# Kernel tuning notes

Measured on AMD Instinct MI355X. Metric: run time of the kernel, lower is better.

Reference implementation:

```python
import jax, jax.numpy as jnp
import numpy as np

# BQQ block dims: Y_sign (p,j,k,m,l), Z_sign (p,j,k,l,n); in=k*n=4096, out=j*m=4096
P, J, K, M, L, N = 2, 32, 32, 128, 16, 128
ACT_BITS = 8  # activation quantization bits


def setup_inputs() -> dict:
    key = jax.random.key(0)
    ks = jax.random.split(key, 7)
    x = jax.random.normal(ks[0], (1, 512, K * N), dtype=jnp.float32)
    # sign matrices in {-1,+1}
    Y_sign = jnp.where(jax.random.normal(ks[1], (P, J, K, M, L)) >= 0, 1.0, -1.0).astype(jnp.float32)
    Z_sign = jnp.where(jax.random.normal(ks[2], (P, J, K, L, N)) >= 0, 1.0, -1.0).astype(jnp.float32)
    # per-block positive scales (abs-mean in the original, so strictly > 0)
    Y_scale = jax.random.uniform(ks[3], (P, J, K, 1, 1), minval=0.01, maxval=0.1, dtype=jnp.float32)
    Z_scale = jax.random.uniform(ks[4], (P, J, K, 1, 1), minval=0.01, maxval=0.1, dtype=jnp.float32)
    A = jax.random.normal(ks[5], (P, J, K, 4), dtype=jnp.float32) * 0.1
    bias = jax.random.normal(ks[6], (J * M,), dtype=jnp.float32) * 0.1
    return {"input": x, "Y_sign": Y_sign, "Z_sign": Z_sign,
            "Y_scale": Y_scale, "Z_scale": Z_scale, "A": A, "bias": bias}


def reference(input, Y_sign, Z_sign, Y_scale, Z_scale, A, bias):
    # --- activation quantization (act_bits = 8, simple round, no STE) ---
    qmax = float(2 ** (ACT_BITS - 1) - 1)  # 127
    x_max = jnp.max(input)
    x_min = jnp.min(input)
    act_scale = jnp.maximum((x_max - x_min) / (2.0 * qmax), 1e-8)
    X = jnp.clip(jnp.round(input / act_scale), -qmax, qmax) * act_scale

    # --- dequantize sign * scale ---
    Y_q = Y_sign * Y_scale  # (p,j,k,m,l)
    Z_q = Z_sign * Z_scale  # (p,j,k,l,n)

    orig_shape = X.shape[:-1]
    X_kn = X.reshape(-1, K, N)  # (B,k,n)

    # chained block einsums
    T = jnp.einsum('bkn,pjkln->bpjkl', X_kn, Z_q)          # (B,p,j,k,l)
    core = jnp.einsum('pjkml,bpjkl->bpjkm', Y_q, T)        # (B,p,j,k,m)

    # quant_bias=True correction terms: A[...,0..3] = (a,b,c,d)
    out1 = jnp.einsum('bpjkm,pjk->bjm', core, A[..., 0])

    Y_sum = Y_q.sum(axis=-1)                               # (p,j,k,m)
    B_coef = jnp.einsum('pjk,pjkm->jkm', A[..., 1], Y_sum)
    Sx = X_kn.sum(axis=-1)                                 # (B,k)
    out2 = jnp.einsum('bk,jkm->bjm', Sx, B_coef)

    Zs = Z_q.sum(axis=-2)                                  # (p,j,k,n)
    Tz = jnp.einsum('bkn,pjkn->bpjk', X_kn, Zs)
    out3 = jnp.einsum('bpjk,pjk->bj', Tz, A[..., 2])

    D_coef = A[..., 3].sum(axis=0)                         # (j,k)
    out4 = jnp.einsum('bk,jk->bj', Sx, D_coef)

    out_bjm = out1 + out2 + (out3 + out4)[:, :, None]      # (B,j,m)
    out_2d = out_bjm.reshape(-1, J * M) + bias
    return out_2d.reshape(*orig_shape, J * M)
```

## Files before the change

kernel.cpp:

```cpp
#include <hip/hip_runtime.h>
#include <hip/hip_bf16.h>

typedef __attribute__((ext_vector_type(4))) float f32x4;
typedef __attribute__((ext_vector_type(8))) short bf16x8;

#define GLOBAL_AS __attribute__((address_space(1)))
#define LDS_AS __attribute__((address_space(3)))

static __device__ __forceinline__ unsigned short f2bf(float f) {
  __hip_bfloat16 h = __float2bfloat16(f);
  return __builtin_bit_cast(unsigned short, h);
}
static __device__ __forceinline__ float bf2f(unsigned short u) {
  unsigned int v = ((unsigned int)u) << 16;
  return __builtin_bit_cast(float, v);
}
static __device__ __forceinline__ void load_lds16(const void* g, void* l) {
  __builtin_amdgcn_global_load_lds((GLOBAL_AS void*)g, (LDS_AS void*)l, 16, 0, 0);
}

__global__ __launch_bounds__(256) void k_minmax_part(const float* __restrict__ x,
                                                     float* __restrict__ part) {
  int tid = blockIdx.x * 256 + threadIdx.x;
  const float4* xv = (const float4*)x;
  float mn = 3.4e38f, mx = -3.4e38f;
#pragma unroll
  for (int rep = 0; rep < 8; ++rep) {
    float4 v = xv[tid + rep * 65536];
    mn = fminf(mn, fminf(fminf(v.x, v.y), fminf(v.z, v.w)));
    mx = fmaxf(mx, fmaxf(fmaxf(v.x, v.y), fmaxf(v.z, v.w)));
  }
#pragma unroll
  for (int o = 32; o > 0; o >>= 1) {
    mn = fminf(mn, __shfl_down(mn, o));
    mx = fmaxf(mx, __shfl_down(mx, o));
  }
  __shared__ float smn[4], smx[4];
  int lane = threadIdx.x & 63, w = threadIdx.x >> 6;
  if (lane == 0) { smn[w] = mn; smx[w] = mx; }
  __syncthreads();
  if (threadIdx.x == 0) {
    mn = fminf(fminf(smn[0], smn[1]), fminf(smn[2], smn[3]));
    mx = fmaxf(fmaxf(smx[0], smx[1]), fmaxf(smx[2], smx[3]));
    part[2 * blockIdx.x] = mn;
    part[2 * blockIdx.x + 1] = mx;
  }
}

__global__ __launch_bounds__(256) void k_fused(const float* __restrict__ x,
                                               const float* __restrict__ part,
                                               const float* __restrict__ Ysg,
                                               const float* __restrict__ Zsg,
                                               const float* __restrict__ Ysc,
                                               const float* __restrict__ Zsc,
                                               const float* __restrict__ Acoef,
                                               float* __restrict__ scl,
                                               unsigned short* __restrict__ xq,
                                               unsigned short* __restrict__ W) {
  const int t = threadIdx.x;
  if (blockIdx.x < 1024) {
    const int jk = blockIdx.x;
    __shared__ float Yl[32][128];
    __shared__ float Zl[32][128];
    __shared__ float B1[128], C1[128];
    __shared__ float cf[7];
    if (t < 2) {
      int idx = t * 1024 + jk;
      float ys = Ysc[idx], zs = Zsc[idx];
      cf[t] = Acoef[idx * 4 + 0] * ys * zs;
      cf[2 + t] = Acoef[idx * 4 + 1] * ys;
      cf[4 + t] = Acoef[idx * 4 + 2] * zs;
    } else if (t == 2) {
      cf[6] = Acoef[jk * 4 + 3] + Acoef[(1024 + jk) * 4 + 3];
    }
#pragma unroll
    for (int rep = 0; rep < 4; ++rep) {
      int q = t + rep * 256;
      int p = q >> 9, m = (q >> 2) & 127, l0 = (q & 3) * 4;
      float4 v = *(const float4*)(Ysg + (size_t)(p * 1024 + jk) * 2048 + m * 16 + l0);
      Yl[p * 16 + l0 + 0][m] = v.x;
      Yl[p * 16 + l0 + 1][m] = v.y;
      Yl[p * 16 + l0 + 2][m] = v.z;
      Yl[p * 16 + l0 + 3][m] = v.w;
    }
#pragma unroll
    for (int rep = 0; rep < 4; ++rep) {
      int q = t + rep * 256;
      int p = q >> 9, l = (q >> 5) & 15, n0 = (q & 31) * 4;
      float4 v = *(const float4*)(Zsg + (size_t)(p * 1024 + jk) * 2048 + l * 128 + n0);
      *(float4*)&Zl[p * 16 + l][n0] = v;
    }
    __syncthreads();
    if (t < 128) {
      float s = 0.f;
#pragma unroll
      for (int pl = 0; pl < 32; ++pl) s += cf[2 + (pl >> 4)] * Yl[pl][t];
      B1[t] = s;
    } else {
      int n = t - 128;
      float s = 0.f;
#pragma unroll
      for (int pl = 0; pl < 32; ++pl) s += cf[4 + (pl >> 4)] * Zl[pl][n];
      C1[n] = s;
    }
    __syncthreads();
    const int m0 = (t >> 3) * 4;
    const int n0 = (t & 7) * 4;
    float acc[4][16];
#pragma unroll
    for (int i = 0; i < 4; ++i)
#pragma unroll
      for (int g = 0; g < 16; ++g) acc[i][g] = 0.f;
    for (int pl = 0; pl < 32; ++pl) {
      float c = cf[pl >> 4];
      float4 y = *(const float4*)&Yl[pl][m0];
      float ym[4] = {y.x * c, y.y * c, y.z * c, y.w * c};
      float zr[16];
#pragma unroll
      for (int g = 0; g < 4; ++g) {
        float4 z = *(const float4*)&Zl[pl][n0 + g * 32];
        zr[g * 4 + 0] = z.x; zr[g * 4 + 1] = z.y; zr[g * 4 + 2] = z.z; zr[g * 4 + 3] = z.w;
      }
#pragma unroll
      for (int i = 0; i < 4; ++i)
#pragma unroll
        for (int g = 0; g < 16; ++g) acc[i][g] = fmaf(ym[i], zr[g], acc[i][g]);
    }
    const int j = jk >> 5, k = jk & 31;
    const float Dv = cf[6];
#pragma unroll
    for (int i = 0; i < 4; ++i) {
      int m = m0 + i;
      float bm = B1[m] + Dv;
      size_t rowoff = (size_t)(j * 128 + m) * 4096 + (size_t)(k * 128);
#pragma unroll
      for (int g = 0; g < 4; ++g) {
        int n = n0 + g * 32;
        ushort4 o = make_ushort4(f2bf(acc[i][g * 4 + 0] + bm + C1[n + 0]),
                                 f2bf(acc[i][g * 4 + 1] + bm + C1[n + 1]),
                                 f2bf(acc[i][g * 4 + 2] + bm + C1[n + 2]),
                                 f2bf(acc[i][g * 4 + 3] + bm + C1[n + 3]));
        *(ushort4*)(W + rowoff + n) = o;
      }
    }
  } else {
    const int qb = blockIdx.x - 1024;
    float2 v2 = ((const float2*)part)[t];
    float mn = v2.x, mx = v2.y;
#pragma unroll
    for (int o = 32; o > 0; o >>= 1) {
      mn = fminf(mn, __shfl_down(mn, o));
      mx = fmaxf(mx, __shfl_down(mx, o));
    }
    __shared__ float smn2[4], smx2[4], ssc[1];
    int lane = t & 63, w = t >> 6;
    if (lane == 0) { smn2[w] = mn; smx2[w] = mx; }
    __syncthreads();
    if (t == 0) {
      mn = fminf(fminf(smn2[0], smn2[1]), fminf(smn2[2], smn2[3]));
      mx = fmaxf(fmaxf(smx2[0], smx2[1]), fmaxf(smx2[2], smx2[3]));
      ssc[0] = fmaxf((mx - mn) / 254.0f, 1e-8f);
      if (qb == 0) scl[0] = ssc[0];
    }
    __syncthreads();
    const float s = ssc[0];
    int i = qb * 256 + t;
    float4 v = ((const float4*)x)[i];
    float a = fminf(fmaxf(rintf(v.x / s), -127.f), 127.f);
    float b = fminf(fmaxf(rintf(v.y / s), -127.f), 127.f);
    float c = fminf(fmaxf(rintf(v.z / s), -127.f), 127.f);
    float d = fminf(fmaxf(rintf(v.w / s), -127.f), 127.f);
    ((ushort4*)xq)[i] = make_ushort4(f2bf(a), f2bf(b), f2bf(c), f2bf(d));
  }
}

__global__ __launch_bounds__(512) void k_gemm(const unsigned short* __restrict__ Xq,
                                              const unsigned short* __restrict__ W,
                                              float* __restrict__ out,
                                              unsigned short* __restrict__ P) {
  __shared__ unsigned short Al[3][256 * 64];
  __shared__ unsigned short Bl[3][128 * 64];
  const int t = threadIdx.x, lane = t & 63, wid = t >> 6;
  const int wg = (blockIdx.x & 7) * 32 + (blockIdx.x >> 3);
  const int bn = wg >> 3;
  const int sk = (wg >> 1) & 3;
  const int bm = wg & 1;
  const int wm = wid >> 1, wn = wid & 1;
  const int kbase = sk * 1024;
  f32x4 acc[4][4];
#pragma unroll
  for (int a = 0; a < 4; ++a)
#pragma unroll
    for (int b = 0; b < 4; ++b) acc[a][b] = (f32x4)(0.f);

  const int lr = lane >> 3;
  const int lcb = (lane & 7) * 16;

  auto STAGE = [&](int buf, int kt) {
    const int k0 = kbase + kt * 64;
#pragma unroll
    for (int c = 0; c < 4; ++c) {
      int chunk = wid * 4 + c;
      int r = chunk * 8 + lr;
      int colb = lcb ^ ((r & 7) << 4);
      load_lds16(Xq + ((size_t)(bm * 256 + r) << 12) + k0 + (colb >> 1), &Al[buf][chunk * 512]);
    }
#pragma unroll
    for (int c = 0; c < 2; ++c) {
      int chunk = wid * 2 + c;
      int r = chunk * 8 + lr;
      int colb = lcb ^ ((r & 7) << 4);
      load_lds16(W + ((size_t)(bn * 128 + r) << 12) + k0 + (colb >> 1), &Bl[buf][chunk * 512]);
    }
  };

  auto COMPUTE = [&](int buf) {
#pragma unroll
    for (int ks = 0; ks < 2; ++ks) {
      bf16x8 af[4], bfr[4];
#pragma unroll
      for (int fm = 0; fm < 4; ++fm) {
        int r = wm * 64 + fm * 16 + (lane & 15);
        int colb = (ks * 64 + ((lane >> 4) * 16)) ^ ((r & 7) << 4);
        af[fm] = *(const bf16x8*)((const char*)&Al[buf][0] + r * 128 + colb);
      }
#pragma unroll
      for (int fn = 0; fn < 4; ++fn) {
        int r = wn * 64 + fn * 16 + (lane & 15);
        int colb = (ks * 64 + ((lane >> 4) * 16)) ^ ((r & 7) << 4);
        bfr[fn] = *(const bf16x8*)((const char*)&Bl[buf][0] + r * 128 + colb);
      }
#pragma unroll
      for (int fm = 0; fm < 4; ++fm)
#pragma unroll
        for (int fn = 0; fn < 4; ++fn)
          acc[fm][fn] = __builtin_amdgcn_mfma_f32_16x16x32_bf16(af[fm], bfr[fn], acc[fm][fn], 0, 0, 0);
    }
  };

  STAGE(0, 0);
  STAGE(1, 1);
  int b0 = 2;
  for (int it = 0; it < 16; ++it) {
    STAGE(b0, (it + 2) & 15);
    __builtin_amdgcn_sched_barrier(0);
    asm volatile("s_waitcnt vmcnt(12)" ::: "memory");
    __builtin_amdgcn_sched_barrier(0);
    __builtin_amdgcn_s_barrier();
    __builtin_amdgcn_sched_barrier(0);
    int cb = b0 + 1;
    if (cb >= 3) cb -= 3;
    COMPUTE(cb);
    __builtin_amdgcn_sched_barrier(0);
    __builtin_amdgcn_s_barrier();
    b0 = cb;
  }

  if (sk == 0) {
#pragma unroll
    for (int fn = 0; fn < 4; ++fn) {
      int col = bn * 128 + wn * 64 + fn * 16 + (lane & 15);
#pragma unroll
      for (int fm = 0; fm < 4; ++fm) {
#pragma unroll
        for (int i = 0; i < 4; ++i) {
          int row = bm * 256 + wm * 64 + fm * 16 + (lane >> 4) * 4 + i;
          out[(size_t)row * 4096 + col] = acc[fm][fn][i];
        }
      }
    }
  } else {
    unsigned short* Pk = P + (size_t)(sk - 1) * 2097152;
#pragma unroll
    for (int fn = 0; fn < 4; ++fn) {
      int col = bn * 128 + wn * 64 + fn * 16 + (lane & 15);
#pragma unroll
      for (int fm = 0; fm < 4; ++fm) {
#pragma unroll
        for (int i = 0; i < 4; ++i) {
          int row = bm * 256 + wm * 64 + fm * 16 + (lane >> 4) * 4 + i;
          Pk[(size_t)row * 4096 + col] = f2bf(acc[fm][fn][i]);
        }
      }
    }
  }
}

__global__ __launch_bounds__(256) void k_epi(float* __restrict__ out,
                                             const unsigned short* __restrict__ P,
                                             const float* __restrict__ scl,
                                             const float* __restrict__ bias) {
  int i4 = blockIdx.x * 256 + threadIdx.x;
  const float s = scl[0];
  float4 r = ((const float4*)out)[i4];
  float4 bv = ((const float4*)bias)[i4 & 1023];
  float sx = r.x, sy = r.y, sz = r.z, sw = r.w;
#pragma unroll
  for (int k = 0; k < 3; ++k) {
    ushort4 p = ((const ushort4*)(P + (size_t)k * 2097152))[i4];
    sx += bf2f(p.x); sy += bf2f(p.y); sz += bf2f(p.z); sw += bf2f(p.w);
  }
  ((float4*)out)[i4] = make_float4(sx * s + bv.x, sy * s + bv.y, sz * s + bv.z, sw * s + bv.w);
}

__global__ __launch_bounds__(512) void k_gemm_fb(const unsigned short* __restrict__ Xq,
                                                 const unsigned short* __restrict__ W,
                                                 const float* __restrict__ scl,
                                                 const float* __restrict__ bias,
                                                 float* __restrict__ out) {
  __shared__ unsigned short Al[4][128 * 64];
  __shared__ unsigned short Bl[4][64 * 64];
  const int t = threadIdx.x, lane = t & 63, wid = t >> 6;
  const int wg = (blockIdx.x & 7) * 32 + (blockIdx.x >> 3);
  const int bm = wg & 3;
  const int bn = wg >> 2;
  const int wm = wid >> 1, wn = wid & 1;
  f32x4 acc[2][2];
#pragma unroll
  for (int a = 0; a < 2; ++a)
#pragma unroll
    for (int b = 0; b < 2; ++b) acc[a][b] = (f32x4)(0.f);
  const int lr = lane >> 3;
  const int lcb = (lane & 7) * 16;
  auto STAGE = [&](int buf, int kt) {
    const int k0 = kt * 64;
#pragma unroll
    for (int c = 0; c < 2; ++c) {
      int chunk = wid * 2 + c;
      int r = chunk * 8 + lr;
      int colb = lcb ^ ((r & 7) << 4);
      load_lds16(Xq + ((size_t)(bm * 128 + r) << 12) + k0 + (colb >> 1), &Al[buf][chunk * 512]);
    }
    {
      int r = wid * 8 + lr;
      int colb = lcb ^ ((r & 7) << 4);
      load_lds16(W + ((size_t)(bn * 64 + r) << 12) + k0 + (colb >> 1), &Bl[buf][wid * 512]);
    }
  };
  auto COMPUTE = [&](int buf) {
#pragma unroll
    for (int ks = 0; ks < 2; ++ks) {
      bf16x8 af[2], bfr[2];
#pragma unroll
      for (int fm = 0; fm < 2; ++fm) {
        int r = wm * 32 + fm * 16 + (lane & 15);
        int colb = (ks * 64 + ((lane >> 4) * 16)) ^ ((r & 7) << 4);
        af[fm] = *(const bf16x8*)((const char*)&Al[buf][0] + r * 128 + colb);
      }
#pragma unroll
      for (int fn = 0; fn < 2; ++fn) {
        int r = wn * 32 + fn * 16 + (lane & 15);
        int colb = (ks * 64 + ((lane >> 4) * 16)) ^ ((r & 7) << 4);
        bfr[fn] = *(const bf16x8*)((const char*)&Bl[buf][0] + r * 128 + colb);
      }
#pragma unroll
      for (int fm = 0; fm < 2; ++fm)
#pragma unroll
        for (int fn = 0; fn < 2; ++fn)
          acc[fm][fn] = __builtin_amdgcn_mfma_f32_16x16x32_bf16(af[fm], bfr[fn], acc[fm][fn], 0, 0, 0);
    }
  };
  STAGE(0, 0); STAGE(1, 1); STAGE(2, 2);
  for (int t64 = 0; t64 < 64; ++t64) {
    STAGE((t64 + 3) & 3, (t64 + 3) & 63);
    __builtin_amdgcn_sched_barrier(0);
    asm volatile("s_waitcnt vmcnt(9)" ::: "memory");
    __builtin_amdgcn_sched_barrier(0);
    __builtin_amdgcn_s_barrier();
    __builtin_amdgcn_sched_barrier(0);
    COMPUTE(t64 & 3);
    __builtin_amdgcn_sched_barrier(0);
    __builtin_amdgcn_s_barrier();
  }
  const float s = scl[0];
#pragma unroll
  for (int fn = 0; fn < 2; ++fn) {
    int col = bn * 64 + wn * 32 + fn * 16 + (lane & 15);
    float bv = bias[col];
#pragma unroll
    for (int fm = 0; fm < 2; ++fm) {
#pragma unroll
      for (int i = 0; i < 4; ++i) {
        int row = bm * 128 + wm * 32 + fm * 16 + (lane >> 4) * 4 + i;
        out[(size_t)row * 4096 + col] = acc[fm][fn][i] * s + bv;
      }
    }
  }
}

extern "C" void kernel_launch(void* const* d_in, const int* in_sizes, int n_in,
                              void* d_out, int out_size, void* d_ws, size_t ws_size,
                              hipStream_t stream) {
  const float* x    = (const float*)d_in[0];
  const float* Ysg  = (const float*)d_in[1];
  const float* Zsg  = (const float*)d_in[2];
  const float* Ysc  = (const float*)d_in[3];
  const float* Zsc  = (const float*)d_in[4];
  const float* A    = (const float*)d_in[5];
  const float* bias = (const float*)d_in[6];
  float* out = (float*)d_out;

  char* ws = (char*)d_ws;
  float* scl  = (float*)ws;
  float* part = (float*)(ws + 256);
  unsigned short* Xq = (unsigned short*)(ws + 65536);
  unsigned short* W  = (unsigned short*)(ws + 65536 + (size_t)4194304);
  unsigned short* P  = (unsigned short*)(ws + 65536 + (size_t)4194304 + (size_t)33554432);

  k_minmax_part<<<dim3(256), dim3(256), 0, stream>>>(x, part);
  k_fused<<<dim3(3072), dim3(256), 0, stream>>>(x, part, Ysg, Zsg, Ysc, Zsc, A, scl, Xq, W);
  if (ws_size >= (size_t)65536 + 4194304 + 33554432 + 12582912) {
    k_gemm<<<dim3(256), dim3(512), 0, stream>>>(Xq, W, out, P);
    k_epi<<<dim3(2048), dim3(256), 0, stream>>>(out, P, scl, bias);
  } else {
    k_gemm_fb<<<dim3(256), dim3(512), 0, stream>>>(Xq, W, scl, bias, out);
  }
}
```

Baseline: 65.19 us.

## Build weight blocks with bf16 MFMA and fuse row sums into loads

The per-block 128x128 weight tile, a rank-32 product of scaled sign matrices, was computed with scalar FMAs from fp32 LDS. It is now built with bf16 MFMA 16x16x32 instructions, with Y and Z staged in padded bf16 LDS layouts, and the Y row sums are taken with shuffles during the load. This cuts LDS footprint and FMA work in the weight-build phase. The cost is scattered 2-byte output stores instead of vectorized ushort4 stores, and rounding Y times its coefficient to bf16 before the product.

```diff
diff --git a/kernel.cpp b/kernel.cpp
--- a/kernel.cpp
+++ b/kernel.cpp
@@ -3,6 +3,7 @@
 
 typedef __attribute__((ext_vector_type(4))) float f32x4;
 typedef __attribute__((ext_vector_type(8))) short bf16x8;
+typedef __attribute__((ext_vector_type(4))) unsigned int u32x4;
 
 #define GLOBAL_AS __attribute__((address_space(1)))
 #define LDS_AS __attribute__((address_space(3)))
@@ -60,87 +61,96 @@
   const int t = threadIdx.x;
   if (blockIdx.x < 1024) {
     const int jk = blockIdx.x;
-    __shared__ float Yl[32][128];
-    __shared__ float Zl[32][128];
-    __shared__ float B1[128], C1[128];
-    __shared__ float cf[7];
-    if (t < 2) {
-      int idx = t * 1024 + jk;
-      float ys = Ysc[idx], zs = Zsc[idx];
-      cf[t] = Acoef[idx * 4 + 0] * ys * zs;
-      cf[2 + t] = Acoef[idx * 4 + 1] * ys;
-      cf[4 + t] = Acoef[idx * 4 + 2] * zs;
-    } else if (t == 2) {
-      cf[6] = Acoef[jk * 4 + 3] + Acoef[(1024 + jk) * 4 + 3];
+    __shared__ unsigned short Yb[2 * 128 * 24];
+    __shared__ unsigned short Zb[128 * 36];
+    __shared__ float B1p[2][128];
+    __shared__ float C1[128];
+    float cf0[2], cf2[2], cf4[2];
+    float Dv;
+    {
+      float ys0 = Ysc[jk], zs0 = Zsc[jk], ys1 = Ysc[1024 + jk], zs1 = Zsc[1024 + jk];
+      const float* A0p = Acoef + (size_t)jk * 4;
+      const float* A1p = Acoef + (size_t)(1024 + jk) * 4;
+      cf0[0] = A0p[0] * ys0 * zs0; cf0[1] = A1p[0] * ys1 * zs1;
+      cf2[0] = A0p[1] * ys0;       cf2[1] = A1p[1] * ys1;
+      cf4[0] = A0p[2] * zs0;       cf4[1] = A1p[2] * zs1;
+      Dv = A0p[3] + A1p[3];
     }
 #pragma unroll
     for (int rep = 0; rep < 4; ++rep) {
-      int q = t + rep * 256;
-      int p = q >> 9, m = (q >> 2) & 127, l0 = (q & 3) * 4;
+      int q = rep * 256 + t;
+      int l0 = (q & 3) * 4, m = (q >> 2) & 127, p = q >> 9;
       float4 v = *(const float4*)(Ysg + (size_t)(p * 1024 + jk) * 2048 + m * 16 + l0);
-      Yl[p * 16 + l0 + 0][m] = v.x;
-      Yl[p * 16 + l0 + 1][m] = v.y;
-      Yl[p * 16 + l0 + 2][m] = v.z;
-      Yl[p * 16 + l0 + 3][m] = v.w;
+      float s4 = v.x + v.y + v.z + v.w;
+      s4 += __shfl_xor(s4, 1);
+      s4 += __shfl_xor(s4, 2);
+      if ((t & 3) == 0) B1p[p][m] = s4;
+      float c0 = cf0[p];
+      ushort4 o = make_ushort4(f2bf(c0 * v.x), f2bf(c0 * v.y), f2bf(c0 * v.z), f2bf(c0 * v.w));
+      *(ushort4*)&Yb[(p * 128 + m) * 24 + l0] = o;
     }
 #pragma unroll
     for (int rep = 0; rep < 4; ++rep) {
-      int q = t + rep * 256;
-      int p = q >> 9, l = (q >> 5) & 15, n0 = (q & 31) * 4;
+      int q = rep * 256 + t;
+      int n0 = (q & 31) * 4, l = (q >> 5) & 15, p = q >> 9;
       float4 v = *(const float4*)(Zsg + (size_t)(p * 1024 + jk) * 2048 + l * 128 + n0);
-      *(float4*)&Zl[p * 16 + l][n0] = v;
+      int pl = p * 16 + l;
+      Zb[(n0 + 0) * 36 + pl] = f2bf(v.x);
+      Zb[(n0 + 1) * 36 + pl] = f2bf(v.y);
+      Zb[(n0 + 2) * 36 + pl] = f2bf(v.z);
+      Zb[(n0 + 3) * 36 + pl] = f2bf(v.w);
     }
     __syncthreads();
     if (t < 128) {
-      float s = 0.f;
-#pragma unroll
-      for (int pl = 0; pl < 32; ++pl) s += cf[2 + (pl >> 4)] * Yl[pl][t];
-      B1[t] = s;
-    } else {
-      int n = t - 128;
-      float s = 0.f;
-#pragma unroll
-      for (int pl = 0; pl < 32; ++pl) s += cf[4 + (pl >> 4)] * Zl[pl][n];
-      C1[n] = s;
+      float s0 = 0.f, s1 = 0.f;
+#pragma unroll
+      for (int l = 0; l < 16; ++l) {
+        s0 += bf2f(Zb[t * 36 + l]);
+        s1 += bf2f(Zb[t * 36 + 16 + l]);
+      }
+      C1[t] = cf4[0] * s0 + cf4[1] * s1;
     }
     __syncthreads();
-    const int m0 = (t >> 3) * 4;
-    const int n0 = (t & 7) * 4;
-    float acc[4][16];
-#pragma unroll
-    for (int i = 0; i < 4; ++i)
-#pragma unroll
-      for (int g = 0; g < 16; ++g) acc[i][g] = 0.f;
-    for (int pl = 0; pl < 32; ++pl) {
-      float c = cf[pl >> 4];
-      float4 y = *(const float4*)&Yl[pl][m0];
-      float ym[4] = {y.x * c, y.y * c, y.z * c, y.w * c};
-      float zr[16];
-#pragma unroll
-      for (int g = 0; g < 4; ++g) {
-        float4 z = *(const float4*)&Zl[pl][n0 + g * 32];
-        zr[g * 4 + 0] = z.x; zr[g * 4 + 1] = z.y; zr[g * 4 + 2] = z.z; zr[g * 4 + 3] = z.w;
-      }
-#pragma unroll
-      for (int i = 0; i < 4; ++i)
-#pragma unroll
-        for (int g = 0; g < 16; ++g) acc[i][g] = fmaf(ym[i], zr[g], acc[i][g]);
-    }
+    const int lane = t & 63, wid = t >> 6;
+    const int wm = wid >> 1, wn = wid & 1;
+    const int grp = lane >> 4;
+    bf16x8 af[4], bfr[4];
+#pragma unroll
+    for (int fm = 0; fm < 4; ++fm) {
+      int m = wm * 64 + fm * 16 + (lane & 15);
+      af[fm] = *(const bf16x8*)((const char*)Yb + ((grp >> 1) * 128 + m) * 48 + (grp & 1) * 16);
+    }
+#pragma unroll
+    for (int fn = 0; fn < 4; ++fn) {
+      int n = wn * 64 + fn * 16 + (lane & 15);
+      const char* zp = (const char*)Zb + n * 72 + grp * 16;
+      uint2 z0 = *(const uint2*)zp;
+      uint2 z1 = *(const uint2*)(zp + 8);
+      u32x4 zw; zw[0] = z0.x; zw[1] = z0.y; zw[2] = z1.x; zw[3] = z1.y;
+      bfr[fn] = __builtin_bit_cast(bf16x8, zw);
+    }
+    f32x4 acc[4][4];
+#pragma unroll
+    for (int fm = 0; fm < 4; ++fm)
+#pragma unroll
+      for (int fn = 0; fn < 4; ++fn)
+        acc[fm][fn] = __builtin_amdgcn_mfma_f32_16x16x32_bf16(af[fm], bfr[fn], (f32x4)(0.f), 0, 0, 0);
     const int j = jk >> 5, k = jk & 31;
-    const float Dv = cf[6];
-#pragma unroll
-    for (int i = 0; i < 4; ++i) {
-      int m = m0 + i;
-      float bm = B1[m] + Dv;
-      size_t rowoff = (size_t)(j * 128 + m) * 4096 + (size_t)(k * 128);
-#pragma unroll
-      for (int g = 0; g < 4; ++g) {
-        int n = n0 + g * 32;
-        ushort4 o = make_ushort4(f2bf(acc[i][g * 4 + 0] + bm + C1[n + 0]),
-                                 f2bf(acc[i][g * 4 + 1] + bm + C1[n + 1]),
-                                 f2bf(acc[i][g * 4 + 2] + bm + C1[n + 2]),
-                                 f2bf(acc[i][g * 4 + 3] + bm + C1[n + 3]));
-        *(ushort4*)(W + rowoff + n) = o;
+    float c1v[4];
+#pragma unroll
+    for (int fn = 0; fn < 4; ++fn) c1v[fn] = C1[wn * 64 + fn * 16 + (lane & 15)];
+#pragma unroll
+    for (int fm = 0; fm < 4; ++fm) {
+#pragma unroll
+      for (int i = 0; i < 4; ++i) {
+        int row = wm * 64 + fm * 16 + (grp)*4 + i;
+        float b1v = cf2[0] * B1p[0][row] + cf2[1] * B1p[1][row] + Dv;
+        size_t rowoff = (size_t)(j * 128 + row) * 4096 + (size_t)(k * 128);
+#pragma unroll
+        for (int fn = 0; fn < 4; ++fn) {
+          int col = wn * 64 + fn * 16 + (lane & 15);
+          W[rowoff + col] = f2bf(acc[fm][fn][i] + b1v + c1v[fn]);
+        }
       }
     }
   } else {
```

Result: faster. 56.93 us (-12.7%).
